# Optimization experiments

Measured on AMD Instinct MI355X. Metric: run time of the kernel, lower is better.

Reference implementation:

```python
import jax, jax.numpy as jnp
import numpy as np

B, C_IN, N = 4, 64, 4096
E = 131072          # number of edges (avg degree 32)
C_OUT = 63          # out_channels - 1 because add_counts=True


def setup_inputs() -> dict:
    key = jax.random.key(0)
    k1, k2, k3, k4, k5 = jax.random.split(key, 5)
    x = jax.random.normal(k1, (B, C_IN, N), dtype=jnp.float32)
    adj_indices = jax.random.randint(k2, (2, E), 0, N, dtype=jnp.int64)
    adj_values = jax.random.uniform(k3, (E,), dtype=jnp.float32) * 12.0  # cart distances
    W = jax.random.normal(k4, (C_OUT, C_IN, 2), dtype=jnp.float32) * 0.05  # Conv1d weight (k=2)
    b = jax.random.normal(k5, (C_OUT,), dtype=jnp.float32) * 0.05
    return {"x": x, "adj_indices": adj_indices, "adj_values": adj_values, "W": W, "b": b}


def reference(x, adj_indices, adj_values, W, b):
    # Sparse equivalent of: adj_pw = expand_adjacency_tensor(adj).to_dense();
    # x @ adj_pw.T -> Conv1d(k=2, s=2) -> @ adj_pw[::2].
    n = x.shape[2]
    src = adj_indices[0]  # row 2k of adj_pw
    dst = adj_indices[1]  # row 2k+1 of adj_pw
    # Gather endpoint features: [B, C_in, E] each.
    xi = x[:, :, src]
    xj = x[:, :, dst]
    # Conv1d kernel=2 stride=2 over interleaved (src, dst) pairs == per-edge mix.
    out = (jnp.einsum('bce,oc->boe', xi, W[:, :, 0])
           + jnp.einsum('bce,oc->boe', xj, W[:, :, 1])
           + b[None, :, None])  # [B, C_out, E]
    # Scatter-add edge messages back to source nodes (adj_pw[::2]).
    y = jnp.zeros((x.shape[0], W.shape[0], n), dtype=x.dtype).at[:, :, src].add(out)
    # adj.to_dense().sum(dim=0): column sums of adjacency values.
    adj_sum = jax.ops.segment_sum(adj_values, dst, num_segments=n)  # [N]
    # normalize=True: divide by clamped column sums.
    denom = jnp.where(adj_sum == 0, jnp.ones_like(adj_sum), adj_sum)
    y = y / denom[None, None, :]
    # add_counts=True: append adj_sum as an extra channel.
    counts = jnp.broadcast_to(adj_sum[None, None, :], (x.shape[0], 1, n))
    return jnp.concatenate([y, counts], axis=1)  # [B, 64, N]
```

## Files before the change

### kernel.cpp

```cpp
#include <hip/hip_runtime.h>

#define BATCH   4
#define CIN     64
#define NNODES  4096
#define NEDGES  131072
#define COUT    63
#define NPB     16
#define CAP     128
#define GROUPS  256
#define GSHIFT  4
#define PBLK    256
#define SEGCAP  16
#define SEGSH   4

__global__ __launch_bounds__(1024) void k_prep(
    const float* __restrict__ x,
    const int* __restrict__ src,
    const int* __restrict__ dst,
    const float* __restrict__ vals,
    float* __restrict__ xT,
    int* __restrict__ sgb,
    int2* __restrict__ dgb,
    int* __restrict__ scnt,
    int* __restrict__ dcnt)
{
    __shared__ float tile[64][65];
    __shared__ union BB {
        int  s[GROUPS][SEGCAP];
        int2 d[GROUPS][SEGCAP];
    } bb;
    __shared__ int bcnt[GROUPS];

    const int blk = blockIdx.x;
    const int tid = threadIdx.x;
    const int w = tid >> 6, lane = tid & 63;

    int s_ = 0, d_ = 0; float v_ = 0.f;
    const bool hasE = tid < 512;
    if (hasE) {
        int e = blk * 512 + tid;
        s_ = src[e]; d_ = dst[e]; v_ = vals[e];
    }

    if (tid < GROUPS) bcnt[tid] = 0;
    __syncthreads();
    if (hasE) {
        int g = s_ >> GSHIFT;
        int p = atomicAdd(&bcnt[g], 1);
        if (p < SEGCAP) bb.s[g][p] = ((s_ & (NPB - 1)) << 12) | d_;
    }
    __syncthreads();
#pragma unroll
    for (int it = 0; it < GROUPS / 16; ++it) {
        int g = w * 16 + it;
        int sc = min(bcnt[g], SEGCAP);
        if (lane < sc) sgb[((size_t)(g * PBLK + blk) << SEGSH) + lane] = bb.s[g][lane];
        if (lane == 0) scnt[g * PBLK + blk] = sc;
    }
    __syncthreads();

    if (tid < GROUPS) bcnt[tid] = 0;
    __syncthreads();
    if (hasE) {
        int g = d_ >> GSHIFT;
        int q = atomicAdd(&bcnt[g], 1);
        if (q < SEGCAP) bb.d[g][q] = make_int2(d_ & (NPB - 1), __float_as_int(v_));
    }
    __syncthreads();
#pragma unroll
    for (int it = 0; it < GROUPS / 16; ++it) {
        int g = w * 16 + it;
        int dc = min(bcnt[g], SEGCAP);
        if (lane < dc) dgb[((size_t)(g * PBLK + blk) << SEGSH) + lane] = bb.d[g][lane];
        if (lane == 0) dcnt[g * PBLK + blk] = dc;
    }

    int b = blk >> 6;
    int n0 = (blk & 63) << 6;
    int tx = tid & 63, ty = tid >> 6;
    const float* xb = x + (size_t)b * CIN * NNODES;
#pragma unroll
    for (int c = ty; c < 64; c += 16)
        tile[c][tx] = xb[(size_t)c * NNODES + n0 + tx];
    __syncthreads();
#pragma unroll
    for (int n = ty; n < 64; n += 16)
        xT[((size_t)(n0 + n) * BATCH + b) * 64 + tx] = tile[tx][n];
}

__global__ __launch_bounds__(1024, 2) void k_main(
    const float* __restrict__ xT,
    const int* __restrict__ sgb,
    const int2* __restrict__ dgb,
    const int* __restrict__ scnt,
    const int* __restrict__ dcnt,
    const float* __restrict__ W,
    const float* __restrict__ bias,
    float* __restrict__ out)
{
    __shared__ float w0s[64][65];
    __shared__ float w1s[64][65];
    __shared__ float aggs[NPB][260];
    __shared__ union U {
        int   lists[NPB][CAP];
        float res[BATCH][64][17];
    } u;
    __shared__ int   lcnt[NPB];
    __shared__ float adjs[NPB];
    __shared__ int   scn[PBLK], dcn[PBLK];

    const int tid   = threadIdx.x;
    const int g     = blockIdx.x;
    const int nbase = g * NPB;
    const int wv    = tid >> 6;
    const int lane  = tid & 63;
    const int n     = nbase + wv;

    if (tid < NPB) { lcnt[tid] = 0; adjs[tid] = 0.f; }
    if (tid < PBLK) {
        scn[tid] = scnt[g * PBLK + tid];
        dcn[tid] = dcnt[g * PBLK + tid];
    }
    {
        const float2* W2 = reinterpret_cast<const float2*>(W);
#pragma unroll
        for (int i = tid; i < COUT * CIN; i += 1024) {
            float2 v = W2[i];
            int o = i >> 6, c = i & 63;
            w0s[c][o] = v.x;
            w1s[c][o] = v.y;
        }
        if (tid < 64) { w0s[tid][63] = 0.f; w1s[tid][63] = 0.f; }
    }
    __syncthreads();

#pragma unroll 1
    for (int i = tid; i < PBLK * SEGCAP; i += 1024) {
        int seg = i >> SEGSH, k = i & (SEGCAP - 1);
        if (k < scn[seg]) {
            int e = sgb[((size_t)g * PBLK << SEGSH) + i];
            int a = e >> 12;
            int p = atomicAdd(&lcnt[a], 1);
            if (p < CAP) u.lists[a][p] = e & 0xFFF;
        }
    }
#pragma unroll 1
    for (int i = tid; i < PBLK * SEGCAP; i += 1024) {
        int seg = i >> SEGSH, k = i & (SEGCAP - 1);
        if (k < dcn[seg]) {
            int2 e = dgb[((size_t)g * PBLK << SEGSH) + i];
            atomicAdd(&adjs[e.x], __int_as_float(e.y));
        }
    }
    __syncthreads();

    const int cnt = lcnt[wv];
    {
        const int k1 = min(cnt, CAP);
        const int* L = u.lists[wv];
        const float* xb = xT + (size_t)lane * 4;
        float4 accA = make_float4(0.f, 0.f, 0.f, 0.f);
        float4 accB = make_float4(0.f, 0.f, 0.f, 0.f);
        int k = 0;
        for (; k + 8 <= k1; k += 8) {
            float4 v0 = *reinterpret_cast<const float4*>(xb + (size_t)L[k + 0] * 256);
            float4 v1 = *reinterpret_cast<const float4*>(xb + (size_t)L[k + 1] * 256);
            float4 v2 = *reinterpret_cast<const float4*>(xb + (size_t)L[k + 2] * 256);
            float4 v3 = *reinterpret_cast<const float4*>(xb + (size_t)L[k + 3] * 256);
            float4 v4 = *reinterpret_cast<const float4*>(xb + (size_t)L[k + 4] * 256);
            float4 v5 = *reinterpret_cast<const float4*>(xb + (size_t)L[k + 5] * 256);
            float4 v6 = *reinterpret_cast<const float4*>(xb + (size_t)L[k + 6] * 256);
            float4 v7 = *reinterpret_cast<const float4*>(xb + (size_t)L[k + 7] * 256);
            accA.x += (v0.x + v1.x) + (v2.x + v3.x);
            accA.y += (v0.y + v1.y) + (v2.y + v3.y);
            accA.z += (v0.z + v1.z) + (v2.z + v3.z);
            accA.w += (v0.w + v1.w) + (v2.w + v3.w);
            accB.x += (v4.x + v5.x) + (v6.x + v7.x);
            accB.y += (v4.y + v5.y) + (v6.y + v7.y);
            accB.z += (v4.z + v5.z) + (v6.z + v7.z);
            accB.w += (v4.w + v5.w) + (v6.w + v7.w);
        }
        for (; k < k1; ++k) {
            float4 v = *reinterpret_cast<const float4*>(xb + (size_t)L[k] * 256);
            accA.x += v.x; accA.y += v.y; accA.z += v.z; accA.w += v.w;
        }
        accA.x += accB.x; accA.y += accB.y; accA.z += accB.z; accA.w += accB.w;
        *reinterpret_cast<float4*>(&aggs[wv][lane * 4]) = accA;
    }
    __syncthreads();

    {
        int o = lane;
        float bval = (o < COUT) ? bias[o] : 0.f;
        const float* xrow = xT + (size_t)n * 256;

        float acc0[4] = {0.f, 0.f, 0.f, 0.f};
        float acc1[4] = {0.f, 0.f, 0.f, 0.f};

#pragma unroll 1
        for (int c4 = 0; c4 < 64; c4 += 4) {
            float w00 = w0s[c4 + 0][o], w01 = w0s[c4 + 1][o];
            float w02 = w0s[c4 + 2][o], w03 = w0s[c4 + 3][o];
            float w10 = w1s[c4 + 0][o], w11 = w1s[c4 + 1][o];
            float w12 = w1s[c4 + 2][o], w13 = w1s[c4 + 3][o];
#pragma unroll
            for (int b = 0; b < 4; ++b) {
                float4 xv = *reinterpret_cast<const float4*>(xrow + b * 64 + c4);
                float4 av = *reinterpret_cast<const float4*>(&aggs[wv][b * 64 + c4]);
                acc0[b] += w00 * xv.x + w01 * xv.y + w02 * xv.z + w03 * xv.w;
                acc1[b] += w10 * av.x + w11 * av.y + w12 * av.z + w13 * av.w;
            }
        }

        float dg = (float)cnt;
        float aj = adjs[wv];
        float rd = 1.f / ((aj == 0.f) ? 1.f : aj);
#pragma unroll
        for (int b = 0; b < 4; ++b) {
            float v = (o < COUT) ? (dg * (acc0[b] + bval) + acc1[b]) * rd : aj;
            u.res[b][o][wv] = v;
        }
    }
    __syncthreads();

#pragma unroll
    for (int i = tid; i < BATCH * 64 * NPB; i += 1024) {
        int b = i >> 10, o = (i >> 4) & 63, nl = i & 15;
        out[((size_t)(b * 64 + o)) * NNODES + nbase + nl] = u.res[b][o][nl];
    }
}

extern "C" void kernel_launch(void* const* d_in, const int* in_sizes, int n_in,
                              void* d_out, int out_size, void* d_ws, size_t ws_size,
                              hipStream_t stream) {
    const float* x    = (const float*)d_in[0];
    const int*   adj  = (const int*)d_in[1];
    const float* vals = (const float*)d_in[2];
    const float* W    = (const float*)d_in[3];
    const float* bias = (const float*)d_in[4];
    float* out = (float*)d_out;

    const int* src = adj;
    const int* dst = adj + NEDGES;

    char* ws = (char*)d_ws;
    float* xT   = (float*)(ws);
    int*   sgb  = (int*)  (ws + (4 << 20));
    int2*  dgb  = (int2*) (ws + (8 << 20));
    int*   scnt = (int*)  (ws + (16 << 20));
    int*   dcnt = (int*)  (ws + (16 << 20) + (256 << 10));

    k_prep<<<BATCH * (NNODES / 64), 1024, 0, stream>>>(x, src, dst, vals,
                                                       xT, sgb, dgb, scnt, dcnt);
    k_main<<<NNODES / NPB, 1024, 0, stream>>>(xT, sgb, dgb, scnt, dcnt,
                                              W, bias, out);
}
```

Measured before the change: 39.08 us.

## Halve nodes per block and split gather and GEMV across two waves per node

Each k_main block now handles 8 nodes instead of 16, so twice as many blocks are launched. Each pair of sibling blocks re-reads the same 16-node bucket segments and filters to its half. Within a block, two wavefronts share each node: the neighbor gather interleaves the edge list between them, and the per-node channel mix is split by batch pairs. The goal is more parallelism and shorter per-wave dependency chains, at the cost of redundant bucket reads, repeated W staging per block, and a higher launch-bounds occupancy hint that may constrain registers.

```diff
diff --git a/kernel.cpp b/kernel.cpp
--- a/kernel.cpp
+++ b/kernel.cpp
@@ -5,9 +5,10 @@
 #define NNODES  4096
 #define NEDGES  131072
 #define COUT    63
-#define NPB     16
+#define NPB     8
 #define CAP     128
 #define GROUPS  256
+#define GNODES  16
 #define GSHIFT  4
 #define PBLK    256
 #define SEGCAP  16
@@ -47,7 +48,7 @@
     if (hasE) {
         int g = s_ >> GSHIFT;
         int p = atomicAdd(&bcnt[g], 1);
-        if (p < SEGCAP) bb.s[g][p] = ((s_ & (NPB - 1)) << 12) | d_;
+        if (p < SEGCAP) bb.s[g][p] = ((s_ & (GNODES - 1)) << 12) | d_;
     }
     __syncthreads();
 #pragma unroll
@@ -64,7 +65,7 @@
     if (hasE) {
         int g = d_ >> GSHIFT;
         int q = atomicAdd(&bcnt[g], 1);
-        if (q < SEGCAP) bb.d[g][q] = make_int2(d_ & (NPB - 1), __float_as_int(v_));
+        if (q < SEGCAP) bb.d[g][q] = make_int2(d_ & (GNODES - 1), __float_as_int(v_));
     }
     __syncthreads();
 #pragma unroll
@@ -88,7 +89,7 @@
         xT[((size_t)(n0 + n) * BATCH + b) * 64 + tx] = tile[tx][n];
 }
 
-__global__ __launch_bounds__(1024, 2) void k_main(
+__global__ __launch_bounds__(1024, 8) void k_main(
     const float* __restrict__ xT,
     const int* __restrict__ sgb,
     const int2* __restrict__ dgb,
@@ -100,21 +101,22 @@
 {
     __shared__ float w0s[64][65];
     __shared__ float w1s[64][65];
-    __shared__ float aggs[NPB][260];
+    __shared__ float aggs[NPB][2][260];
     __shared__ union U {
         int   lists[NPB][CAP];
-        float res[BATCH][64][17];
+        float res[BATCH][64][9];
     } u;
     __shared__ int   lcnt[NPB];
     __shared__ float adjs[NPB];
     __shared__ int   scn[PBLK], dcn[PBLK];
 
     const int tid   = threadIdx.x;
-    const int g     = blockIdx.x;
-    const int nbase = g * NPB;
+    const int blk   = blockIdx.x;
+    const int g     = blk >> 1;
+    const int half8 = (blk & 1) * NPB;
+    const int nbase = blk * NPB;
     const int wv    = tid >> 6;
     const int lane  = tid & 63;
-    const int n     = nbase + wv;
 
     if (tid < NPB) { lcnt[tid] = 0; adjs[tid] = 0.f; }
     if (tid < PBLK) {
@@ -139,9 +141,11 @@
         int seg = i >> SEGSH, k = i & (SEGCAP - 1);
         if (k < scn[seg]) {
             int e = sgb[((size_t)g * PBLK << SEGSH) + i];
-            int a = e >> 12;
-            int p = atomicAdd(&lcnt[a], 1);
-            if (p < CAP) u.lists[a][p] = e & 0xFFF;
+            unsigned a = (unsigned)((e >> 12) - half8);
+            if (a < NPB) {
+                int p = atomicAdd(&lcnt[a], 1);
+                if (p < CAP) u.lists[a][p] = e & 0xFFF;
+            }
         }
     }
 #pragma unroll 1
@@ -149,53 +153,48 @@
         int seg = i >> SEGSH, k = i & (SEGCAP - 1);
         if (k < dcn[seg]) {
             int2 e = dgb[((size_t)g * PBLK << SEGSH) + i];
-            atomicAdd(&adjs[e.x], __int_as_float(e.y));
-        }
-    }
-    __syncthreads();
-
-    const int cnt = lcnt[wv];
+            unsigned a = (unsigned)(e.x - half8);
+            if (a < NPB) atomicAdd(&adjs[a], __int_as_float(e.y));
+        }
+    }
+    __syncthreads();
+
     {
-        const int k1 = min(cnt, CAP);
-        const int* L = u.lists[wv];
+        const int nl = wv >> 1, h = wv & 1;
+        const int k1 = min(lcnt[nl], CAP);
+        const int* L = u.lists[nl];
         const float* xb = xT + (size_t)lane * 4;
         float4 accA = make_float4(0.f, 0.f, 0.f, 0.f);
         float4 accB = make_float4(0.f, 0.f, 0.f, 0.f);
-        int k = 0;
-        for (; k + 8 <= k1; k += 8) {
+        int k = h;
+        for (; k + 6 < k1; k += 8) {
             float4 v0 = *reinterpret_cast<const float4*>(xb + (size_t)L[k + 0] * 256);
-            float4 v1 = *reinterpret_cast<const float4*>(xb + (size_t)L[k + 1] * 256);
-            float4 v2 = *reinterpret_cast<const float4*>(xb + (size_t)L[k + 2] * 256);
-            float4 v3 = *reinterpret_cast<const float4*>(xb + (size_t)L[k + 3] * 256);
-            float4 v4 = *reinterpret_cast<const float4*>(xb + (size_t)L[k + 4] * 256);
-            float4 v5 = *reinterpret_cast<const float4*>(xb + (size_t)L[k + 5] * 256);
-            float4 v6 = *reinterpret_cast<const float4*>(xb + (size_t)L[k + 6] * 256);
-            float4 v7 = *reinterpret_cast<const float4*>(xb + (size_t)L[k + 7] * 256);
-            accA.x += (v0.x + v1.x) + (v2.x + v3.x);
-            accA.y += (v0.y + v1.y) + (v2.y + v3.y);
-            accA.z += (v0.z + v1.z) + (v2.z + v3.z);
-            accA.w += (v0.w + v1.w) + (v2.w + v3.w);
-            accB.x += (v4.x + v5.x) + (v6.x + v7.x);
-            accB.y += (v4.y + v5.y) + (v6.y + v7.y);
-            accB.z += (v4.z + v5.z) + (v6.z + v7.z);
-            accB.w += (v4.w + v5.w) + (v6.w + v7.w);
-        }
-        for (; k < k1; ++k) {
+            float4 v1 = *reinterpret_cast<const float4*>(xb + (size_t)L[k + 2] * 256);
+            float4 v2 = *reinterpret_cast<const float4*>(xb + (size_t)L[k + 4] * 256);
+            float4 v3 = *reinterpret_cast<const float4*>(xb + (size_t)L[k + 6] * 256);
+            accA.x += v0.x + v1.x; accA.y += v0.y + v1.y;
+            accA.z += v0.z + v1.z; accA.w += v0.w + v1.w;
+            accB.x += v2.x + v3.x; accB.y += v2.y + v3.y;
+            accB.z += v2.z + v3.z; accB.w += v2.w + v3.w;
+        }
+        for (; k < k1; k += 2) {
             float4 v = *reinterpret_cast<const float4*>(xb + (size_t)L[k] * 256);
             accA.x += v.x; accA.y += v.y; accA.z += v.z; accA.w += v.w;
         }
         accA.x += accB.x; accA.y += accB.y; accA.z += accB.z; accA.w += accB.w;
-        *reinterpret_cast<float4*>(&aggs[wv][lane * 4]) = accA;
+        *reinterpret_cast<float4*>(&aggs[nl][h][lane * 4]) = accA;
     }
     __syncthreads();
 
     {
-        int o = lane;
+        const int nl = wv >> 1, bp = wv & 1;
+        const int n  = nbase + nl;
+        const int o  = lane;
         float bval = (o < COUT) ? bias[o] : 0.f;
-        const float* xrow = xT + (size_t)n * 256;
-
-        float acc0[4] = {0.f, 0.f, 0.f, 0.f};
-        float acc1[4] = {0.f, 0.f, 0.f, 0.f};
+        const float* xrow = xT + (size_t)n * 256 + bp * 128;
+
+        float acc0[2] = {0.f, 0.f};
+        float acc1[2] = {0.f, 0.f};
 
 #pragma unroll 1
         for (int c4 = 0; c4 < 64; c4 += 4) {
@@ -204,28 +203,33 @@
             float w10 = w1s[c4 + 0][o], w11 = w1s[c4 + 1][o];
             float w12 = w1s[c4 + 2][o], w13 = w1s[c4 + 3][o];
 #pragma unroll
-            for (int b = 0; b < 4; ++b) {
-                float4 xv = *reinterpret_cast<const float4*>(xrow + b * 64 + c4);
-                float4 av = *reinterpret_cast<const float4*>(&aggs[wv][b * 64 + c4]);
-                acc0[b] += w00 * xv.x + w01 * xv.y + w02 * xv.z + w03 * xv.w;
-                acc1[b] += w10 * av.x + w11 * av.y + w12 * av.z + w13 * av.w;
+            for (int j = 0; j < 2; ++j) {
+                int boff = (bp * 2 + j) * 64 + c4;
+                float4 xv = *reinterpret_cast<const float4*>(xrow + j * 64 + c4);
+                float4 a0 = *reinterpret_cast<const float4*>(&aggs[nl][0][boff]);
+                float4 a1 = *reinterpret_cast<const float4*>(&aggs[nl][1][boff]);
+                float avx = a0.x + a1.x, avy = a0.y + a1.y;
+                float avz = a0.z + a1.z, avw = a0.w + a1.w;
+                acc0[j] += w00 * xv.x + w01 * xv.y + w02 * xv.z + w03 * xv.w;
+                acc1[j] += w10 * avx + w11 * avy + w12 * avz + w13 * avw;
             }
         }
 
-        float dg = (float)cnt;
-        float aj = adjs[wv];
+        float dg = (float)lcnt[nl];
+        float aj = adjs[nl];
         float rd = 1.f / ((aj == 0.f) ? 1.f : aj);
 #pragma unroll
-        for (int b = 0; b < 4; ++b) {
-            float v = (o < COUT) ? (dg * (acc0[b] + bval) + acc1[b]) * rd : aj;
-            u.res[b][o][wv] = v;
+        for (int j = 0; j < 2; ++j) {
+            int b = bp * 2 + j;
+            float v = (o < COUT) ? (dg * (acc0[j] + bval) + acc1[j]) * rd : aj;
+            u.res[b][o][nl] = v;
         }
     }
     __syncthreads();
 
 #pragma unroll
     for (int i = tid; i < BATCH * 64 * NPB; i += 1024) {
-        int b = i >> 10, o = (i >> 4) & 63, nl = i & 15;
+        int b = i >> 9, o = (i >> 3) & 63, nl = i & 7;
         out[((size_t)(b * 64 + o)) * NNODES + nbase + nl] = u.res[b][o][nl];
     }
 }
```

Measured after the change: 40.22 us. +2.9%, slower.

## Pre-reduce adjacency column sums per block instead of bucketing dst edges

Applied to the files above, without the earlier changes.

The prep kernel no longer buckets (dst, value) pairs into segmented lists. Each block now accumulates values into a dense shared array of per-node partial sums and writes out 256x16 floats per block. The main kernel then reads 4096 contiguous partials per group, reduces them in registers and does one shared atomic per thread. This removes the count array, the variable-length segment reads and most shared atomics. In exchange it always writes and reads a dense 4 MB partial buffer, even though most entries are zero.

```diff
diff --git a/kernel.cpp b/kernel.cpp
--- a/kernel.cpp
+++ b/kernel.cpp
@@ -20,14 +20,13 @@
     const float* __restrict__ vals,
     float* __restrict__ xT,
     int* __restrict__ sgb,
-    int2* __restrict__ dgb,
-    int* __restrict__ scnt,
-    int* __restrict__ dcnt)
+    float* __restrict__ pdj,
+    int* __restrict__ scnt)
 {
     __shared__ float tile[64][65];
     __shared__ union BB {
-        int  s[GROUPS][SEGCAP];
-        int2 d[GROUPS][SEGCAP];
+        int   s[GROUPS][SEGCAP];
+        float p[GROUPS][NPB];
     } bb;
     __shared__ int bcnt[GROUPS];
 
@@ -59,21 +58,15 @@
     }
     __syncthreads();
 
-    if (tid < GROUPS) bcnt[tid] = 0;
-    __syncthreads();
-    if (hasE) {
-        int g = d_ >> GSHIFT;
-        int q = atomicAdd(&bcnt[g], 1);
-        if (q < SEGCAP) bb.d[g][q] = make_int2(d_ & (NPB - 1), __float_as_int(v_));
-    }
-    __syncthreads();
-#pragma unroll
-    for (int it = 0; it < GROUPS / 16; ++it) {
-        int g = w * 16 + it;
-        int dc = min(bcnt[g], SEGCAP);
-        if (lane < dc) dgb[((size_t)(g * PBLK + blk) << SEGSH) + lane] = bb.d[g][lane];
-        if (lane == 0) dcnt[g * PBLK + blk] = dc;
-    }
+#pragma unroll
+    for (int i = tid; i < GROUPS * NPB; i += 1024)
+        bb.p[i >> 4][i & 15] = 0.f;
+    __syncthreads();
+    if (hasE) atomicAdd(&bb.p[d_ >> GSHIFT][d_ & (NPB - 1)], v_);
+    __syncthreads();
+#pragma unroll
+    for (int i = tid; i < GROUPS * NPB; i += 1024)
+        pdj[((size_t)(i >> 4) * PBLK + blk) * NPB + (i & 15)] = bb.p[i >> 4][i & 15];
 
     int b = blk >> 6;
     int n0 = (blk & 63) << 6;
@@ -91,9 +84,8 @@
 __global__ __launch_bounds__(1024, 2) void k_main(
     const float* __restrict__ xT,
     const int* __restrict__ sgb,
-    const int2* __restrict__ dgb,
+    const float* __restrict__ pdj,
     const int* __restrict__ scnt,
-    const int* __restrict__ dcnt,
     const float* __restrict__ W,
     const float* __restrict__ bias,
     float* __restrict__ out)
@@ -107,7 +99,7 @@
     } u;
     __shared__ int   lcnt[NPB];
     __shared__ float adjs[NPB];
-    __shared__ int   scn[PBLK], dcn[PBLK];
+    __shared__ int   scn[PBLK];
 
     const int tid   = threadIdx.x;
     const int g     = blockIdx.x;
@@ -117,10 +109,7 @@
     const int n     = nbase + wv;
 
     if (tid < NPB) { lcnt[tid] = 0; adjs[tid] = 0.f; }
-    if (tid < PBLK) {
-        scn[tid] = scnt[g * PBLK + tid];
-        dcn[tid] = dcnt[g * PBLK + tid];
-    }
+    if (tid < PBLK) scn[tid] = scnt[g * PBLK + tid];
     {
         const float2* W2 = reinterpret_cast<const float2*>(W);
 #pragma unroll
@@ -144,13 +133,12 @@
             if (p < CAP) u.lists[a][p] = e & 0xFFF;
         }
     }
-#pragma unroll 1
-    for (int i = tid; i < PBLK * SEGCAP; i += 1024) {
-        int seg = i >> SEGSH, k = i & (SEGCAP - 1);
-        if (k < dcn[seg]) {
-            int2 e = dgb[((size_t)g * PBLK << SEGSH) + i];
-            atomicAdd(&adjs[e.x], __int_as_float(e.y));
-        }
+    {
+        const float* P = pdj + (size_t)g * PBLK * NPB;
+        float pa = 0.f;
+#pragma unroll
+        for (int j = 0; j < 4; ++j) pa += P[tid + j * 1024];
+        atomicAdd(&adjs[tid & 15], pa);
     }
     __syncthreads();
 
@@ -246,12 +234,11 @@
     char* ws = (char*)d_ws;
     float* xT   = (float*)(ws);
     int*   sgb  = (int*)  (ws + (4 << 20));
-    int2*  dgb  = (int2*) (ws + (8 << 20));
-    int*   scnt = (int*)  (ws + (16 << 20));
-    int*   dcnt = (int*)  (ws + (16 << 20) + (256 << 10));
+    float* pdj  = (float*)(ws + (8 << 20));
+    int*   scnt = (int*)  (ws + (12 << 20));
 
     k_prep<<<BATCH * (NNODES / 64), 1024, 0, stream>>>(x, src, dst, vals,
-                                                       xT, sgb, dgb, scnt, dcnt);
-    k_main<<<NNODES / NPB, 1024, 0, stream>>>(xT, sgb, dgb, scnt, dcnt,
+                                                       xT, sgb, pdj, scnt);
+    k_main<<<NNODES / NPB, 1024, 0, stream>>>(xT, sgb, pdj, scnt,
                                               W, bias, out);
 }
```

Measured after the change: 37.39 us. 1.05x faster.
